# Optimization experiments

Hardware: AMD Instinct MI355X
Metric: run time of the kernel (lower is better)

Reference implementation:

```python
import jax, jax.numpy as jnp
import numpy as np
import math

KSIZE = 4  # ShortConvolution kernel_size
EPS_NORM = 1e-12
EPS_LN = 1e-5


def short_conv(x, w):
    # x: [b, l, c]; w: [c, K] depthwise causal conv + residual (y = conv(pad(x)) + x)
    b, l, c = x.shape
    K = w.shape[1]
    xp = jnp.pad(x, ((0, 0), (K - 1, 0), (0, 0)))
    y = x  # residual term (x[:, :, K-1:] after padding == x)
    for j in range(K):
        y = y + xp[:, j:j + l, :] * w[:, j]
    return y


def l2norm(x):
    # L2-normalize over last dim (interpreting torch.norm as F.normalize intent)
    return x * jax.lax.rsqrt(jnp.sum(x * x, axis=-1, keepdims=True) + EPS_NORM)


def setup_inputs() -> dict:
    key = jax.random.key(0)
    ks = jax.random.split(key, 12)
    b, l, dim = 4, 2048, 1024
    h = 16
    dk = dim // h
    s = 1.0 / math.sqrt(dim)
    inp = {
        "hidden_states": jax.random.normal(ks[0], (b, l, dim), jnp.float32),
        "Wq": jax.random.normal(ks[1], (dim, dim), jnp.float32) * s,
        "Wk": jax.random.normal(ks[2], (dim, dim), jnp.float32) * s,
        "Wv": jax.random.normal(ks[3], (dim, dim), jnp.float32) * s,
        "conv_q": jax.random.normal(ks[4], (dim, KSIZE), jnp.float32) * 0.1,
        "conv_k": jax.random.normal(ks[5], (dim, KSIZE), jnp.float32) * 0.1,
        "conv_v": jax.random.normal(ks[6], (dim, KSIZE), jnp.float32) * 0.1,
        "W_init": jax.random.normal(ks[7], (1, h, dk, dk), jnp.float32) / math.sqrt(dk),
        "ln_gamma": jnp.ones((dk,), jnp.float32),
        "ln_beta": jnp.zeros((dk,), jnp.float32),
        "Wg": jax.random.normal(ks[8], (dim, dim), jnp.float32) * s,
        "Wo": jax.random.normal(ks[9], (dim, dim), jnp.float32) * s,
    }
    return inp


def titans_forward(hidden_states, Wq, Wk, Wv, conv_q, conv_k, conv_v,
                   W_init, ln_gamma, ln_beta, Wg, Wo,
                   num_heads=16, chunk_size=16):
    b, l, dim = hidden_states.shape
    h = num_heads
    dk = dim // h
    cs = chunk_size
    nc = l // cs

    q = l2norm(jax.nn.silu(short_conv(hidden_states @ Wq.T, conv_q)).reshape(b, l, h, dk))
    k = l2norm(jax.nn.silu(short_conv(hidden_states @ Wk.T, conv_k)).reshape(b, l, h, dk))
    v = jax.nn.silu(short_conv(hidden_states @ Wv.T, conv_v)).reshape(b, l, h, dk)

    # chunked layout: [nc, b, cs, h, d]
    qc = q.reshape(b, nc, cs, h, dk).transpose(1, 0, 2, 3, 4)
    kc = k.reshape(b, nc, cs, h, dk).transpose(1, 0, 2, 3, 4)
    vc = v.reshape(b, nc, cs, h, dk).transpose(1, 0, 2, 3, 4)

    mask = jnp.tril(jnp.ones((cs, cs), q.dtype))
    W0 = jnp.broadcast_to(W_init, (b, h, dk, dk))

    def step(W, chunk):
        q_c, k_c, v_c = chunk
        inter = jnp.einsum('bqhk,bhkv->bqhv', q_c, W)
        qk = jnp.einsum('bqhd,bkhd->bhqk', q_c, k_c) * mask
        intra = jnp.einsum('bhqk,bkhv->bqhv', qk, v_c)
        W_new = W + jnp.einsum('bchk,bchv->bhkv', k_c, v_c)
        return W_new, inter + intra

    _, o = jax.lax.scan(step, W0, (qc, kc, vc))  # o: [nc, b, cs, h, dv]
    o = o.transpose(1, 0, 2, 3, 4).reshape(b, l, h, dk)

    # LayerNorm over head_v_dim
    mu = jnp.mean(o, axis=-1, keepdims=True)
    var = jnp.mean((o - mu) ** 2, axis=-1, keepdims=True)
    o = (o - mu) * jax.lax.rsqrt(var + EPS_LN) * ln_gamma + ln_beta

    o = o.reshape(b, l, dim)
    gate = hidden_states @ Wg.T
    return (o * gate) @ Wo.T


def reference(hidden_states, Wq, Wk, Wv, conv_q, conv_k, conv_v,
              W_init, ln_gamma, ln_beta, Wg, Wo):
    return titans_forward(hidden_states, Wq, Wk, Wv, conv_q, conv_k, conv_v,
                          W_init, ln_gamma, ln_beta, Wg, Wo)
```

## Files before the change

### kernel.cpp

```cpp
#include <hip/hip_runtime.h>

#define L 2048
#define DIM 1024
#define ROWS 8192
#define NSEG 16
#define SEG_CHUNKS 8
#define SEG_TOK 128

typedef __attribute__((ext_vector_type(4))) _Float16 v4h;
typedef __attribute__((ext_vector_type(4))) float v4f;
typedef __attribute__((ext_vector_type(8))) short v8s;

#if defined(__HIP_DEVICE_COMPILE__)
#define MFMA_F16_16x16x16(a, b, c) __builtin_amdgcn_mfma_f32_16x16x16f16((a), (b), (c), 0, 0, 0)
#define MFMA_BF16_16x16x32(a, b, c) __builtin_amdgcn_mfma_f32_16x16x32_bf16((a), (b), (c), 0, 0, 0)
#else
#define MFMA_F16_16x16x16(a, b, c) (c)
#define MFMA_BF16_16x16x32(a, b, c) (c)
#endif

__device__ inline void gld16(const unsigned short* g, unsigned short* l) {
#if defined(__HIP_DEVICE_COMPILE__)
  __builtin_amdgcn_global_load_lds(
      (__attribute__((address_space(1))) void*)g,
      (__attribute__((address_space(3))) void*)l, 16, 0, 0);
#endif
}

__device__ inline unsigned short f2bf(float f) {
  unsigned int u = __float_as_uint(f);
  unsigned int r = (u + 0x7fffu + ((u >> 16) & 1u)) >> 16;
  return (unsigned short)r;
}
__device__ inline void u2_unpack(const uint2 u, float* f) {
  f[0] = __uint_as_float((u.x & 0xffffu) << 16);
  f[1] = __uint_as_float(u.x & 0xffff0000u);
  f[2] = __uint_as_float((u.y & 0xffffu) << 16);
  f[3] = __uint_as_float(u.y & 0xffff0000u);
}
__device__ inline uint4 pack8(const float4 a, const float4 b) {
  uint4 u;
  u.x = (unsigned int)f2bf(a.x) | ((unsigned int)f2bf(a.y) << 16);
  u.y = (unsigned int)f2bf(a.z) | ((unsigned int)f2bf(a.w) << 16);
  u.z = (unsigned int)f2bf(b.x) | ((unsigned int)f2bf(b.y) << 16);
  u.w = (unsigned int)f2bf(b.z) | ((unsigned int)f2bf(b.w) << 16);
  return u;
}
__device__ inline unsigned short f2h_us(float f) {
  _Float16 h = (_Float16)f;
  unsigned short u;
  __builtin_memcpy(&u, &h, 2);
  return u;
}
__device__ inline float h2f_us(unsigned short u) {
  _Float16 h;
  __builtin_memcpy(&h, &u, 2);
  return (float)h;
}
__device__ inline void h4_unpack(const uint2 u, float* f) {
  f[0] = h2f_us((unsigned short)(u.x & 0xffffu));
  f[1] = h2f_us((unsigned short)(u.x >> 16));
  f[2] = h2f_us((unsigned short)(u.y & 0xffffu));
  f[3] = h2f_us((unsigned short)(u.y >> 16));
}

__global__ __launch_bounds__(256) void cvt_all(const float* __restrict__ H,
                                               const float* __restrict__ w0,
                                               const float* __restrict__ w1,
                                               const float* __restrict__ w2,
                                               const float* __restrict__ w3,
                                               unsigned short* __restrict__ Hbf,
                                               unsigned short* __restrict__ Wbf) {
  const int i = blockIdx.x * 256 + threadIdx.x;
  const float* s;
  unsigned short* d;
  int li;
  if (i < 2097152) {
    s = H; d = Hbf; li = i;
  } else {
    const int j = i - 2097152;
    const int w = j >> 18;
    li = j & 262143;
    s = (w == 0) ? w0 : (w == 1) ? w1 : (w == 2) ? w2 : w3;
    d = Wbf + (size_t)w * DIM * DIM;
  }
  const float4 v = ((const float4*)s)[li];
  uint2 u;
  u.x = (unsigned int)f2bf(v.x) | ((unsigned int)f2bf(v.y) << 16);
  u.y = (unsigned int)f2bf(v.z) | ((unsigned int)f2bf(v.w) << 16);
  ((uint2*)d)[li] = u;
}

__global__ __launch_bounds__(256) void cvt_f2b(const float* __restrict__ s,
                                               unsigned short* __restrict__ d) {
  const int i = blockIdx.x * 256 + threadIdx.x;
  const float4 v = ((const float4*)s)[i];
  uint2 u;
  u.x = (unsigned int)f2bf(v.x) | ((unsigned int)f2bf(v.y) << 16);
  u.y = (unsigned int)f2bf(v.z) | ((unsigned int)f2bf(v.w) << 16);
  ((uint2*)d)[i] = u;
}

template <int OUTF32>
__global__ __launch_bounds__(256) void gemm_a(const unsigned short* __restrict__ A,
                                              const unsigned short* __restrict__ B,
                                              unsigned short* __restrict__ o0,
                                              unsigned short* __restrict__ o1,
                                              unsigned short* __restrict__ o2,
                                              unsigned short* __restrict__ o3) {
  __shared__ __align__(16) unsigned short As[128 * 64];
  __shared__ __align__(16) unsigned short Bs[128 * 64];
  const int tid = threadIdx.x;
  const int bm = blockIdx.y * 128;
  const int bn = blockIdx.x * 128;
  const int wave = tid >> 6;
  const int lane = tid & 63;
  const int m16 = lane & 15;
  const int g = lane >> 4;
  const int wm = (wave >> 1) * 64;
  const int wn = (wave & 1) * 64;
  const int srow8 = lane >> 3;
  const int schk = lane & 7;

  v4f acc[4][4];
#pragma unroll
  for (int i = 0; i < 4; i++)
#pragma unroll
    for (int j = 0; j < 4; j++) acc[i][j] = (v4f){0.f, 0.f, 0.f, 0.f};

  for (int kt = 0; kt < DIM; kt += 64) {
    __syncthreads();
#pragma unroll
    for (int j = 0; j < 4; j++) {
      const int r = wave * 32 + j * 8 + srow8;
      const int cg = schk ^ (r & 7);
      gld16(A + (size_t)(bm + r) * DIM + kt + cg * 8, &As[(wave * 32 + j * 8) * 64]);
      gld16(B + (size_t)(bn + r) * DIM + kt + cg * 8, &Bs[(wave * 32 + j * 8) * 64]);
    }
    __syncthreads();
#pragma unroll
    for (int kh = 0; kh < 2; kh++) {
      v8s af[4], bf[4];
#pragma unroll
      for (int i = 0; i < 4; i++) {
        const int r = wm + i * 16 + m16;
        af[i] = *(const v8s*)&As[r * 64 + (((kh * 4 + g) ^ (r & 7)) * 8)];
      }
#pragma unroll
      for (int j = 0; j < 4; j++) {
        const int r = wn + j * 16 + m16;
        bf[j] = *(const v8s*)&Bs[r * 64 + (((kh * 4 + g) ^ (r & 7)) * 8)];
      }
#pragma unroll
      for (int i = 0; i < 4; i++)
#pragma unroll
        for (int j = 0; j < 4; j++) acc[i][j] = MFMA_BF16_16x16x32(af[i], bf[j], acc[i][j]);
    }
  }

  const int t = bn >> 10;
  const int cb = bn & 1023;
  unsigned short* C = (t == 0) ? o0 : (t == 1) ? o1 : (t == 2) ? o2 : o3;
#pragma unroll
  for (int i = 0; i < 4; i++)
#pragma unroll
    for (int e = 0; e < 4; e++) {
      const size_t row = (size_t)(bm + wm + i * 16 + 4 * g + e);
#pragma unroll
      for (int j = 0; j < 4; j++) {
        const size_t idx = row * DIM + cb + wn + j * 16 + m16;
        if (OUTF32)
          ((float*)o0)[idx] = acc[i][j][e];
        else
          C[idx] = f2bf(acc[i][j][e]);
      }
    }
}

__global__ __launch_bounds__(256) void gemm_gate(const float* __restrict__ Af,
                                                 const unsigned short* __restrict__ Bf,
                                                 unsigned short* __restrict__ C) {
  __shared__ __align__(16) unsigned short As[128][40];
  __shared__ __align__(16) unsigned short Bs[128][40];
  const int tid = threadIdx.x;
  const int bm = blockIdx.y * 128;
  const int bn = blockIdx.x * 128;
  const int wave = tid >> 6;
  const int lane = tid & 63;
  const int m16 = lane & 15;
  const int g = lane >> 4;
  const int wm = (wave >> 1) * 64;
  const int wn = (wave & 1) * 64;
  const int lr = tid >> 2;
  const int lc = (tid & 3) * 8;

  v4f acc[4][4];
#pragma unroll
  for (int i = 0; i < 4; i++)
#pragma unroll
    for (int j = 0; j < 4; j++) acc[i][j] = (v4f){0.f, 0.f, 0.f, 0.f};

  auto loadAB = [&](int kt, uint4& a0, uint4& a1, uint4& b0, uint4& b1) {
    const float* p0 = Af + (size_t)(bm + lr) * DIM + lc + kt;
    const float* p1 = Af + (size_t)(bm + 64 + lr) * DIM + lc + kt;
    a0 = pack8(*(const float4*)p0, *(const float4*)(p0 + 4));
    a1 = pack8(*(const float4*)p1, *(const float4*)(p1 + 4));
    b0 = *(const uint4*)(Bf + (size_t)(bn + lr) * DIM + lc + kt);
    b1 = *(const uint4*)(Bf + (size_t)(bn + 64 + lr) * DIM + lc + kt);
  };

  uint4 a0, a1, b0, b1;
  loadAB(0, a0, a1, b0, b1);

  for (int kt = 0; kt < DIM; kt += 32) {
    __syncthreads();
    *(uint4*)&As[lr][lc] = a0;
    *(uint4*)&As[64 + lr][lc] = a1;
    *(uint4*)&Bs[lr][lc] = b0;
    *(uint4*)&Bs[64 + lr][lc] = b1;
    __syncthreads();
    if (kt + 32 < DIM) loadAB(kt + 32, a0, a1, b0, b1);
    v8s af[4], bf[4];
#pragma unroll
    for (int i = 0; i < 4; i++) af[i] = *(const v8s*)&As[wm + i * 16 + m16][g * 8];
#pragma unroll
    for (int j = 0; j < 4; j++) bf[j] = *(const v8s*)&Bs[wn + j * 16 + m16][g * 8];
#pragma unroll
    for (int i = 0; i < 4; i++)
#pragma unroll
      for (int j = 0; j < 4; j++) acc[i][j] = MFMA_BF16_16x16x32(af[i], bf[j], acc[i][j]);
  }

#pragma unroll
  for (int i = 0; i < 4; i++)
#pragma unroll
    for (int e = 0; e < 4; e++) {
      const size_t row = (size_t)(bm + wm + i * 16 + 4 * g + e);
#pragma unroll
      for (int j = 0; j < 4; j++)
        C[row * DIM + bn + wn + j * 16 + m16] = f2bf(acc[i][j][e]);
    }
}

__global__ __launch_bounds__(256) void copy_side(const unsigned short* __restrict__ Q,
                                                 const unsigned short* __restrict__ K,
                                                 const unsigned short* __restrict__ V,
                                                 unsigned short* __restrict__ sQ,
                                                 unsigned short* __restrict__ sK,
                                                 unsigned short* __restrict__ sV) {
  const int idx = blockIdx.x;
  const int j = idx % 3;
  const int bs = idx / 3;
  const int seg = bs & 15;
  const int b = bs >> 4;
  const int ch = threadIdx.x * 4;
  const size_t so = ((size_t)(bs * 3 + j)) * DIM + ch;
  if (seg == 0) {
    const uint2 z = {0u, 0u};
    *(uint2*)(sQ + so) = z;
    *(uint2*)(sK + so) = z;
    *(uint2*)(sV + so) = z;
  } else {
    const size_t go = ((size_t)(b * L + seg * SEG_TOK - 3 + j)) * DIM + ch;
    *(uint2*)(sQ + so) = *(const uint2*)(Q + go);
    *(uint2*)(sK + so) = *(const uint2*)(K + go);
    *(uint2*)(sV + so) = *(const uint2*)(V + go);
  }
}

__global__ __launch_bounds__(256) void scan_seg(unsigned short* __restrict__ Qr,
                                                const unsigned short* __restrict__ Kr,
                                                unsigned short* __restrict__ Vr,
                                                const unsigned short* __restrict__ sQ,
                                                const unsigned short* __restrict__ sK,
                                                const unsigned short* __restrict__ sV,
                                                const float* __restrict__ CWq,
                                                const float* __restrict__ CWk,
                                                const float* __restrict__ CWv,
                                                float* __restrict__ D) {
  const int seg = blockIdx.x & 15;
  const int h = (blockIdx.x >> 4) & 15;
  const int b = blockIdx.x >> 8;
  const int tid = threadIdx.x;
  const int lane = tid & 63;
  const int dt = tid >> 6;
  const int m = lane & 15;
  const int g = lane >> 4;
  const int segbase = seg * SEG_TOK;

  __shared__ __align__(16) unsigned short rq[32][68];
  __shared__ __align__(16) unsigned short rk[32][68];
  __shared__ __align__(16) unsigned short rv[32][68];
  __shared__ __align__(16) _Float16 qs[16][72];
  __shared__ __align__(16) _Float16 ks[16][72];
  __shared__ __align__(16) _Float16 kts[64][20];
  __shared__ __align__(16) _Float16 vts[64][20];

  v4f Wf[4];
#pragma unroll
  for (int kt = 0; kt < 4; kt++) Wf[kt] = (v4f){0.f, 0.f, 0.f, 0.f};

  const int srow = tid >> 4;
  const int scol = (tid & 15) * 4;
  const size_t gcol = (size_t)h * 64 + scol;

  float wq[4][4], wk[4][4], wv[4][4];
#pragma unroll
  for (int e = 0; e < 4; e++) {
    const float4 a = *(const float4*)(CWq + (gcol + e) * 4);
    const float4 bw = *(const float4*)(CWk + (gcol + e) * 4);
    const float4 cw = *(const float4*)(CWv + (gcol + e) * 4);
    wq[e][0] = a.x; wq[e][1] = a.y; wq[e][2] = a.z; wq[e][3] = a.w;
    wk[e][0] = bw.x; wk[e][1] = bw.y; wk[e][2] = bw.z; wk[e][3] = bw.w;
    wv[e][0] = cw.x; wv[e][1] = cw.y; wv[e][2] = cw.z; wv[e][3] = cw.w;
  }

  if (tid < 48) {
    const int j = tid >> 4;
    const int sc = (tid & 15) * 4;
    const size_t so = ((size_t)((b * NSEG + seg) * 3 + j)) * DIM + h * 64 + sc;
    const int slot = (29 + j);
    *(uint2*)&rq[slot][sc] = *(const uint2*)(sQ + so);
    *(uint2*)&rk[slot][sc] = *(const uint2*)(sK + so);
    *(uint2*)&rv[slot][sc] = *(const uint2*)(sV + so);
  }

  size_t gb = ((size_t)(b * L + segbase + srow)) * DIM + gcol;
  uint2 qg = *(const uint2*)(Qr + gb);
  uint2 kg = *(const uint2*)(Kr + gb);
  uint2 vg = *(const uint2*)(Vr + gb);

  for (int c = 0; c < SEG_CHUNKS; c++) {
    const int t = segbase + c * 16 + srow;
    __syncthreads();
    *(uint2*)&rq[t & 31][scol] = qg;
    *(uint2*)&rk[t & 31][scol] = kg;
    *(uint2*)&rv[t & 31][scol] = vg;
    const int cn = (c + 1 < SEG_CHUNKS) ? c + 1 : c;
    const size_t gbn = ((size_t)(b * L + segbase + cn * 16 + srow)) * DIM + gcol;
    const uint2 qn = *(const uint2*)(Qr + gbn);
    const uint2 kn = *(const uint2*)(Kr + gbn);
    const uint2 vn = *(const uint2*)(Vr + gbn);
    __syncthreads();

    float sq[4], sk[4], sv[4];
    {
      float q0[4], q1[4], q2[4], q3[4];
      float k0[4], k1[4], k2[4], k3[4];
      float v0[4], v1[4], v2[4], v3[4];
      u2_unpack(qg, q0);
      u2_unpack(kg, k0);
      u2_unpack(vg, v0);
      u2_unpack(*(const uint2*)&rq[(t - 1) & 31][scol], q1);
      u2_unpack(*(const uint2*)&rk[(t - 1) & 31][scol], k1);
      u2_unpack(*(const uint2*)&rv[(t - 1) & 31][scol], v1);
      u2_unpack(*(const uint2*)&rq[(t - 2) & 31][scol], q2);
      u2_unpack(*(const uint2*)&rk[(t - 2) & 31][scol], k2);
      u2_unpack(*(const uint2*)&rv[(t - 2) & 31][scol], v2);
      u2_unpack(*(const uint2*)&rq[(t - 3) & 31][scol], q3);
      u2_unpack(*(const uint2*)&rk[(t - 3) & 31][scol], k3);
      u2_unpack(*(const uint2*)&rv[(t - 3) & 31][scol], v3);
#pragma unroll
      for (int e = 0; e < 4; e++) {
        const float yq = q0[e] + wq[e][0] * q3[e] + wq[e][1] * q2[e] + wq[e][2] * q1[e] + wq[e][3] * q0[e];
        const float yk = k0[e] + wk[e][0] * k3[e] + wk[e][1] * k2[e] + wk[e][2] * k1[e] + wk[e][3] * k0[e];
        const float yv = v0[e] + wv[e][0] * v3[e] + wv[e][1] * v2[e] + wv[e][2] * v1[e] + wv[e][3] * v0[e];
        sq[e] = yq / (1.f + __expf(-yq));
        sk[e] = yk / (1.f + __expf(-yk));
        sv[e] = yv / (1.f + __expf(-yv));
      }
    }
    float ssq = sq[0] * sq[0] + sq[1] * sq[1] + sq[2] * sq[2] + sq[3] * sq[3];
    float ssk = sk[0] * sk[0] + sk[1] * sk[1] + sk[2] * sk[2] + sk[3] * sk[3];
#pragma unroll
    for (int off = 8; off >= 1; off >>= 1) {
      ssq += __shfl_xor(ssq, off, 16);
      ssk += __shfl_xor(ssk, off, 16);
    }
    const float scq = rsqrtf(ssq + 1e-12f);
    const float sck = rsqrtf(ssk + 1e-12f);

    const v4h qh = {(_Float16)(sq[0] * scq), (_Float16)(sq[1] * scq),
                    (_Float16)(sq[2] * scq), (_Float16)(sq[3] * scq)};
    const v4h kh = {(_Float16)(sk[0] * sck), (_Float16)(sk[1] * sck),
                    (_Float16)(sk[2] * sck), (_Float16)(sk[3] * sck)};
    *(v4h*)&qs[srow][scol] = qh;
    *(v4h*)&ks[srow][scol] = kh;
    kts[scol + 0][srow] = kh[0]; kts[scol + 1][srow] = kh[1];
    kts[scol + 2][srow] = kh[2]; kts[scol + 3][srow] = kh[3];
    vts[scol + 0][srow] = (_Float16)sv[0]; vts[scol + 1][srow] = (_Float16)sv[1];
    vts[scol + 2][srow] = (_Float16)sv[2]; vts[scol + 3][srow] = (_Float16)sv[3];

    uint2 qp;
    __builtin_memcpy(&qp, &qh, 8);
    *(uint2*)(Qr + gb) = qp;

    __syncthreads();

    v4h qf[4], kf[4], ktf[4];
#pragma unroll
    for (int kt = 0; kt < 4; kt++) {
      qf[kt] = *(const v4h*)&qs[m][kt * 16 + 4 * g];
      kf[kt] = *(const v4h*)&ks[m][kt * 16 + 4 * g];
      ktf[kt] = *(const v4h*)&kts[kt * 16 + m][4 * g];
    }
    const v4h vf = *(const v4h*)&vts[dt * 16 + m][4 * g];

    v4f kq = {0.f, 0.f, 0.f, 0.f};
#pragma unroll
    for (int kt = 0; kt < 4; kt++) kq = MFMA_F16_16x16x16(kf[kt], qf[kt], kq);

    v4h kqA;
#pragma unroll
    for (int e = 0; e < 4; e++)
      kqA[e] = (4 * g + e <= m) ? (_Float16)kq[e] : (_Float16)0.f;

    v4f of = {0.f, 0.f, 0.f, 0.f};
    of = MFMA_F16_16x16x16(kqA, vf, of);
#pragma unroll
    for (int kt = 0; kt < 4; kt++) {
      v4h Wh;
#pragma unroll
      for (int e = 0; e < 4; e++) Wh[e] = (_Float16)Wf[kt][e];
      of = MFMA_F16_16x16x16(qf[kt], Wh, of);
    }
#pragma unroll
    for (int kt = 0; kt < 4; kt++) Wf[kt] = MFMA_F16_16x16x16(ktf[kt], vf, Wf[kt]);

    const size_t ob = ((size_t)(b * L + segbase + c * 16 + 4 * g)) * DIM + h * 64 + dt * 16 + m;
#pragma unroll
    for (int e = 0; e < 4; e++) Vr[ob + (size_t)e * DIM] = f2h_us(of[e]);

    qg = qn; kg = kn; vg = vn; gb = gbn;
  }

  float* Dp = D + ((size_t)((b * 16 + h) * NSEG + seg)) * 4096;
#pragma unroll
  for (int kt = 0; kt < 4; kt++)
#pragma unroll
    for (int e = 0; e < 4; e++)
      Dp[(kt * 16 + 4 * g + e) * 64 + dt * 16 + m] = Wf[kt][e];
}

__global__ __launch_bounds__(256) void prefix_D(float* __restrict__ D,
                                                const float* __restrict__ W0) {
  const int bh = blockIdx.x;
  const int h = bh & 15;
  const int tid = threadIdx.x;
  float p[16];
#pragma unroll
  for (int i = 0; i < 16; i++) p[i] = W0[(size_t)h * 4096 + tid + i * 256];
  for (int s = 0; s < NSEG; s++) {
    float* Dp = D + ((size_t)bh * NSEG + s) * 4096;
#pragma unroll
    for (int i = 0; i < 16; i++) {
      const float t = Dp[tid + i * 256];
      Dp[tid + i * 256] = p[i];
      p[i] += t;
    }
  }
}

__global__ __launch_bounds__(256) void corr_ln_gate(const unsigned short* __restrict__ Qc,
                                                    const float* __restrict__ P,
                                                    unsigned short* __restrict__ Op,
                                                    const unsigned short* __restrict__ G,
                                                    const float* __restrict__ gamma,
                                                    const float* __restrict__ beta) {
  const int seg = blockIdx.x & 15;
  const int h = (blockIdx.x >> 4) & 15;
  const int b = blockIdx.x >> 8;
  const int tid = threadIdx.x;
  const int lane = tid & 63;
  const int dt = tid >> 6;
  const int m = lane & 15;
  const int g = lane >> 4;

  __shared__ __align__(16) _Float16 Pt[64][72];
  __shared__ __align__(16) _Float16 qt[16][72];
  __shared__ __align__(16) float ot[16][68];

  const float* Pp = P + ((size_t)((b * 16 + h) * NSEG + seg)) * 4096;
#pragma unroll
  for (int i = 0; i < 16; i++) {
    const int el = tid + i * 256;
    Pt[el & 63][el >> 6] = (_Float16)Pp[el];
  }
  __syncthreads();

  v4h pb[4];
#pragma unroll
  for (int kt = 0; kt < 4; kt++) pb[kt] = *(const v4h*)&Pt[dt * 16 + m][kt * 16 + 4 * g];

  const int srow = tid >> 4;
  const int scol = (tid & 15) * 4;
  const float4 gm = *(const float4*)(gamma + scol);
  const float4 bt = *(const float4*)(beta + scol);

  for (int rt = 0; rt < 8; rt++) {
    const int row0 = seg * SEG_TOK + rt * 16;
    const size_t gb = ((size_t)(b * L + row0 + srow)) * DIM + h * 64 + scol;
    const uint2 qg = *(const uint2*)(Qc + gb);
    __syncthreads();
    *(uint2*)&qt[srow][scol] = qg;
    __syncthreads();
    v4h qf[4];
#pragma unroll
    for (int kt = 0; kt < 4; kt++) qf[kt] = *(const v4h*)&qt[m][kt * 16 + 4 * g];
    v4f corr = {0.f, 0.f, 0.f, 0.f};
#pragma unroll
    for (int kt = 0; kt < 4; kt++) corr = MFMA_F16_16x16x16(qf[kt], pb[kt], corr);
    const size_t ob = ((size_t)(b * L + row0 + 4 * g)) * DIM + h * 64 + dt * 16 + m;
#pragma unroll
    for (int e = 0; e < 4; e++)
      ot[4 * g + e][dt * 16 + m] = h2f_us(Op[ob + (size_t)e * DIM]) + corr[e];
    __syncthreads();
    const float4 ov = *(const float4*)&ot[srow][scol];
    float sum = ov.x + ov.y + ov.z + ov.w;
#pragma unroll
    for (int off = 8; off >= 1; off >>= 1) sum += __shfl_xor(sum, off, 16);
    const float mu = sum * (1.f / 64.f);
    const float d0 = ov.x - mu, d1 = ov.y - mu, d2 = ov.z - mu, d3 = ov.w - mu;
    float vs = d0 * d0 + d1 * d1 + d2 * d2 + d3 * d3;
#pragma unroll
    for (int off = 8; off >= 1; off >>= 1) vs += __shfl_xor(vs, off, 16);
    const float rstd = rsqrtf(vs * (1.f / 64.f) + 1e-5f);
    float gt[4];
    u2_unpack(*(const uint2*)(G + gb), gt);
    float outv[4];
    outv[0] = (d0 * rstd * gm.x + bt.x) * gt[0];
    outv[1] = (d1 * rstd * gm.y + bt.y) * gt[1];
    outv[2] = (d2 * rstd * gm.z + bt.z) * gt[2];
    outv[3] = (d3 * rstd * gm.w + bt.w) * gt[3];
    uint2 u;
    u.x = (unsigned int)f2bf(outv[0]) | ((unsigned int)f2bf(outv[1]) << 16);
    u.y = (unsigned int)f2bf(outv[2]) | ((unsigned int)f2bf(outv[3]) << 16);
    *(uint2*)(Op + gb) = u;
  }
}

extern "C" void kernel_launch(void* const* d_in, const int* in_sizes, int n_in,
                              void* d_out, int out_size, void* d_ws, size_t ws_size,
                              hipStream_t stream) {
  const float* H  = (const float*)d_in[0];
  const float* Wq = (const float*)d_in[1];
  const float* Wk = (const float*)d_in[2];
  const float* Wv = (const float*)d_in[3];
  const float* cq = (const float*)d_in[4];
  const float* ck = (const float*)d_in[5];
  const float* cv = (const float*)d_in[6];
  const float* W0 = (const float*)d_in[7];
  const float* gamma = (const float*)d_in[8];
  const float* beta  = (const float*)d_in[9];
  const float* Wg = (const float*)d_in[10];
  const float* Wo = (const float*)d_in[11];

  const size_t SZ = (size_t)ROWS * DIM;
  const size_t WSZ = (size_t)DIM * DIM;
  const size_t SIDE = (size_t)192 * DIM;
  unsigned short* sA = (unsigned short*)d_ws;
  unsigned short* sB = sA + SZ;
  unsigned short* sC = sB + SZ;

  const bool bigws = ws_size >= (3 * SZ + 4 * WSZ + 3 * SIDE) * 2;

  unsigned short* Hbf = (unsigned short*)d_out;
  float* D = (float*)d_out;

  if (bigws) {
    unsigned short* Wbf = sC + SZ;
    unsigned short* side = Wbf + 4 * WSZ;
    unsigned short* gate = Hbf + SZ;

    cvt_all<<<12288, 256, 0, stream>>>(H, Wq, Wk, Wv, Wg, Hbf, Wbf);
    gemm_a<0><<<dim3(32, 64), 256, 0, stream>>>(Hbf, Wbf, sA, sB, sC, gate);
    copy_side<<<192, 256, 0, stream>>>(sA, sB, sC, side, side + SIDE, side + 2 * SIDE);
    scan_seg<<<1024, 256, 0, stream>>>(sA, sB, sC, side, side + SIDE, side + 2 * SIDE,
                                       cq, ck, cv, D);
    prefix_D<<<64, 256, 0, stream>>>(D, W0);
    corr_ln_gate<<<1024, 256, 0, stream>>>(sA, D, sC, gate, gamma, beta);
    cvt_f2b<<<WSZ / 1024, 256, 0, stream>>>(Wo, sA);
    gemm_a<1><<<dim3(8, 64), 256, 0, stream>>>(sC, sA, (unsigned short*)d_out,
                                               nullptr, nullptr, nullptr);
  } else {
    unsigned short* Wbf = Hbf + SZ;
    unsigned short* side = Wbf + 4 * WSZ;

    cvt_all<<<12288, 256, 0, stream>>>(H, Wq, Wk, Wv, Wg, Hbf, Wbf);
    gemm_a<0><<<dim3(24, 64), 256, 0, stream>>>(Hbf, Wbf, sA, sB, sC, nullptr);
    copy_side<<<192, 256, 0, stream>>>(sA, sB, sC, side, side + SIDE, side + 2 * SIDE);
    scan_seg<<<1024, 256, 0, stream>>>(sA, sB, sC, side, side + SIDE, side + 2 * SIDE,
                                       cq, ck, cv, D);
    gemm_gate<<<dim3(8, 64), 256, 0, stream>>>(H, Wbf + 3 * WSZ, sB);
    prefix_D<<<64, 256, 0, stream>>>(D, W0);
    corr_ln_gate<<<1024, 256, 0, stream>>>(sA, D, sC, sB, gamma, beta);
    cvt_f2b<<<WSZ / 1024, 256, 0, stream>>>(Wo, sA);
    gemm_a<1><<<dim3(8, 64), 256, 0, stream>>>(sC, sA, (unsigned short*)d_out,
                                               nullptr, nullptr, nullptr);
  }
}
```

Baseline: 288.4 us.

## Replace QKV+gate projection GEMM with 256x256 tile, 8-wave double-buffered pipelined kernel

```diff
diff --git a/kernel.cpp b/kernel.cpp
--- a/kernel.cpp
+++ b/kernel.cpp
@@ -99,6 +99,165 @@
   u.x = (unsigned int)f2bf(v.x) | ((unsigned int)f2bf(v.y) << 16);
   u.y = (unsigned int)f2bf(v.z) | ((unsigned int)f2bf(v.w) << 16);
   ((uint2*)d)[i] = u;
+}
+
+__global__ __launch_bounds__(512, 2) void gemm8(const unsigned short* __restrict__ A,
+                                                const unsigned short* __restrict__ B,
+                                                unsigned short* __restrict__ o0,
+                                                unsigned short* __restrict__ o1,
+                                                unsigned short* __restrict__ o2,
+                                                unsigned short* __restrict__ o3) {
+  __shared__ __align__(16) unsigned short As[2][256 * 64];
+  __shared__ __align__(16) unsigned short Bs[2][256 * 64];
+  const int tid = threadIdx.x;
+  const int wave = tid >> 6;
+  const int lane = tid & 63;
+  const int m16 = lane & 15;
+  const int g = lane >> 4;
+  const int srow8 = lane >> 3;
+  const int schk = lane & 7;
+  const int wm = wave >> 2;
+  const int wn = wave & 3;
+  const int bm = blockIdx.y * 256;
+  const int bn = blockIdx.x * 256;
+
+  v4f acc[8][4];
+#pragma unroll
+  for (int i = 0; i < 8; i++)
+#pragma unroll
+    for (int j = 0; j < 4; j++) acc[i][j] = (v4f){0.f, 0.f, 0.f, 0.f};
+
+  auto stA = [&](int p, int half, int kt) {
+#pragma unroll
+    for (int j = 0; j < 2; j++) {
+      const int rl = half * 128 + wave * 16 + j * 8;
+      const int r = rl + srow8;
+      const int cg = schk ^ (r & 7);
+      gld16(A + (size_t)(bm + r) * DIM + kt + cg * 8, &As[p][rl * 64]);
+    }
+  };
+  auto stB = [&](int p, int half, int kt) {
+#pragma unroll
+    for (int j = 0; j < 2; j++) {
+      const int rl = half * 128 + wave * 16 + j * 8;
+      const int r = rl + srow8;
+      const int cg = schk ^ (r & 7);
+      gld16(B + (size_t)(bn + r) * DIM + kt + cg * 8, &Bs[p][rl * 64]);
+    }
+  };
+
+  v8s af[2][4], bA[2][2], bB[2][2];
+  auto rdA = [&](const unsigned short* S, int q) {
+#pragma unroll
+    for (int i = 0; i < 4; i++) {
+      const int r = wm * 128 + (q * 4 + i) * 16 + m16;
+#pragma unroll
+      for (int kk = 0; kk < 2; kk++)
+        af[kk][i] = *(const v8s*)&S[r * 64 + ((((kk << 2) + g) ^ (r & 7)) << 3)];
+    }
+  };
+  auto rdB = [&](const unsigned short* S, int nq, v8s (&bf)[2][2]) {
+#pragma unroll
+    for (int j = 0; j < 2; j++) {
+      const int r = wn * 64 + (nq * 2 + j) * 16 + m16;
+#pragma unroll
+      for (int kk = 0; kk < 2; kk++)
+        bf[kk][j] = *(const v8s*)&S[r * 64 + ((((kk << 2) + g) ^ (r & 7)) << 3)];
+    }
+  };
+  auto mma = [&](int mq, int nq, v8s (&bf)[2][2]) {
+#pragma unroll
+    for (int kk = 0; kk < 2; kk++)
+#pragma unroll
+      for (int i = 0; i < 4; i++)
+#pragma unroll
+        for (int j = 0; j < 2; j++)
+          acc[mq * 4 + i][nq * 2 + j] =
+              MFMA_BF16_16x16x32(af[kk][i], bf[kk][j], acc[mq * 4 + i][nq * 2 + j]);
+  };
+
+#define BAR() __builtin_amdgcn_s_barrier()
+#define WAIT_LGKM()                                      \
+  do {                                                   \
+    asm volatile("s_waitcnt lgkmcnt(0)" ::: "memory");   \
+    __builtin_amdgcn_sched_barrier(0);                   \
+  } while (0)
+#define WAIT_VM4() asm volatile("s_waitcnt vmcnt(4)" ::: "memory")
+
+  stA(0, 0, 0); stA(0, 1, 0); stB(0, 0, 0); stB(0, 1, 0);
+  stB(1, 0, 64); stB(1, 1, 64);
+  asm volatile("s_waitcnt vmcnt(4)" ::: "memory");
+  BAR();
+
+  for (int it = 0; it < 8; ++it) {
+    const int kt1 = it * 128 + 64;
+    const int kn0 = (it * 128 + 128 < DIM) ? it * 128 + 128 : 0;
+    const int kn1 = (kt1 + 128 < DIM) ? kt1 + 128 : 0;
+
+    rdA(As[0], 0); rdB(Bs[0], 0, bA);
+    stA(1, 0, kt1);
+    BAR(); WAIT_LGKM();
+    __builtin_amdgcn_s_setprio(1); mma(0, 0, bA); __builtin_amdgcn_s_setprio(0);
+    BAR();
+
+    rdB(Bs[0], 1, bB);
+    stA(1, 1, kt1);
+    BAR(); WAIT_LGKM();
+    __builtin_amdgcn_s_setprio(1); mma(0, 1, bB); __builtin_amdgcn_s_setprio(0);
+    BAR();
+
+    rdA(As[0], 1);
+    stB(0, 0, kn0);
+    BAR(); WAIT_LGKM();
+    __builtin_amdgcn_s_setprio(1); mma(1, 1, bB); __builtin_amdgcn_s_setprio(0);
+    BAR();
+
+    stB(0, 1, kn0);
+    BAR();
+    __builtin_amdgcn_s_setprio(1); mma(1, 0, bA); __builtin_amdgcn_s_setprio(0);
+    WAIT_VM4();
+    BAR();
+
+    rdA(As[1], 0); rdB(Bs[1], 0, bA);
+    stA(0, 0, kn0);
+    BAR(); WAIT_LGKM();
+    __builtin_amdgcn_s_setprio(1); mma(0, 0, bA); __builtin_amdgcn_s_setprio(0);
+    BAR();
+
+    rdB(Bs[1], 1, bB);
+    stA(0, 1, kn0);
+    BAR(); WAIT_LGKM();
+    __builtin_amdgcn_s_setprio(1); mma(0, 1, bB); __builtin_amdgcn_s_setprio(0);
+    BAR();
+
+    rdA(As[1], 1);
+    stB(1, 0, kn1);
+    BAR(); WAIT_LGKM();
+    __builtin_amdgcn_s_setprio(1); mma(1, 1, bB); __builtin_amdgcn_s_setprio(0);
+    BAR();
+
+    stB(1, 1, kn1);
+    BAR();
+    __builtin_amdgcn_s_setprio(1); mma(1, 0, bA); __builtin_amdgcn_s_setprio(0);
+    WAIT_VM4();
+    BAR();
+  }
+
+  const int t = bn >> 10;
+  const int cb = bn & 1023;
+  unsigned short* C = (t == 0) ? o0 : (t == 1) ? o1 : (t == 2) ? o2 : o3;
+#pragma unroll
+  for (int mi = 0; mi < 8; mi++)
+#pragma unroll
+    for (int e = 0; e < 4; e++) {
+      const size_t row = (size_t)(bm + wm * 128 + mi * 16 + 4 * g + e);
+#pragma unroll
+      for (int nj = 0; nj < 4; nj++)
+        C[row * DIM + cb + wn * 64 + nj * 16 + m16] = f2bf(acc[mi][nj][e]);
+    }
+#undef BAR
+#undef WAIT_LGKM
+#undef WAIT_VM4
 }
 
 template <int OUTF32>
@@ -573,7 +732,7 @@
     unsigned short* gate = Hbf + SZ;
 
     cvt_all<<<12288, 256, 0, stream>>>(H, Wq, Wk, Wv, Wg, Hbf, Wbf);
-    gemm_a<0><<<dim3(32, 64), 256, 0, stream>>>(Hbf, Wbf, sA, sB, sC, gate);
+    gemm8<<<dim3(16, 32), 512, 0, stream>>>(Hbf, Wbf, sA, sB, sC, gate);
     copy_side<<<192, 256, 0, stream>>>(sA, sB, sC, side, side + SIDE, side + 2 * SIDE);
     scan_seg<<<1024, 256, 0, stream>>>(sA, sB, sC, side, side + SIDE, side + 2 * SIDE,
                                        cq, ck, cv, D);
@@ -587,7 +746,7 @@
     unsigned short* side = Wbf + 4 * WSZ;
 
     cvt_all<<<12288, 256, 0, stream>>>(H, Wq, Wk, Wv, Wg, Hbf, Wbf);
-    gemm_a<0><<<dim3(24, 64), 256, 0, stream>>>(Hbf, Wbf, sA, sB, sC, nullptr);
+    gemm8<<<dim3(12, 32), 512, 0, stream>>>(Hbf, Wbf, sA, sB, sC, nullptr);
     copy_side<<<192, 256, 0, stream>>>(sA, sB, sC, side, side + SIDE, side + 2 * SIDE);
     scan_seg<<<1024, 256, 0, stream>>>(sA, sB, sC, side, side + SIDE, side + 2 * SIDE,
                                        cq, ck, cv, D);
```

Measured after the change: 286.5 us. Within noise of the previous version (-0.6%).
